# Kernel tuning notes

Measured on AMD Instinct MI355X. Metric: run time of the kernel, lower is better.

## Reference

```python
import jax, jax.numpy as jnp
import numpy as np

B, T, I, H, O = 8192, 512, 4, 32, 4


def setup_inputs() -> dict:
    key = jax.random.key(0)
    ks = jax.random.split(key, 11)
    s = 1.0 / np.sqrt(H)  # PyTorch RNN init scale
    return {
        "X": jax.random.normal(ks[0], (B, T, I), dtype=jnp.float32),
        "W_ih0": jax.random.uniform(ks[1], (H, I), minval=-s, maxval=s, dtype=jnp.float32),
        "W_hh0": jax.random.uniform(ks[2], (H, H), minval=-s, maxval=s, dtype=jnp.float32),
        "b_ih0": jax.random.uniform(ks[3], (H,), minval=-s, maxval=s, dtype=jnp.float32),
        "b_hh0": jax.random.uniform(ks[4], (H,), minval=-s, maxval=s, dtype=jnp.float32),
        "W_ih1": jax.random.uniform(ks[5], (H, H), minval=-s, maxval=s, dtype=jnp.float32),
        "W_hh1": jax.random.uniform(ks[6], (H, H), minval=-s, maxval=s, dtype=jnp.float32),
        "b_ih1": jax.random.uniform(ks[7], (H,), minval=-s, maxval=s, dtype=jnp.float32),
        "b_hh1": jax.random.uniform(ks[8], (H,), minval=-s, maxval=s, dtype=jnp.float32),
        "W_ll": jax.random.uniform(ks[9], (O, H), minval=-s, maxval=s, dtype=jnp.float32),
        "b_ll": jax.random.uniform(ks[10], (O,), minval=-s, maxval=s, dtype=jnp.float32),
    }


def reference(X, W_ih0, W_hh0, b_ih0, b_hh0, W_ih1, W_hh1, b_ih1, b_hh1, W_ll, b_ll):
    # 2-layer tanh RNN (batch_first), zero initial hidden state, then Linear head.
    b0 = b_ih0 + b_hh0
    b1 = b_ih1 + b_hh1
    Bsz = X.shape[0]
    Hdim = W_hh0.shape[0]
    h_init = (jnp.zeros((Bsz, Hdim), X.dtype), jnp.zeros((Bsz, Hdim), X.dtype))

    def step(h, x_t):
        h0, h1 = h
        h0 = jnp.tanh(x_t @ W_ih0.T + h0 @ W_hh0.T + b0)
        h1 = jnp.tanh(h0 @ W_ih1.T + h1 @ W_hh1.T + b1)
        return (h0, h1), h1

    xs = jnp.swapaxes(X, 0, 1)  # [T, B, I]
    _, ys = jax.lax.scan(step, h_init, xs)  # ys: [T, B, H]
    out = ys @ W_ll.T + b_ll  # [T, B, O]
    out = jnp.swapaxes(out, 0, 1)  # [B, T, O]
    return out.reshape(out.shape[0], -1)  # [B, T*O]
```

## Files before the change

### kernel.cpp

```cpp
#include <hip/hip_runtime.h>
#include <cstddef>
#include <cstdint>

constexpr int kB = 8192, kT = 512, kI = 4, kH = 32, kO = 4;

typedef _Float16 f16x8 __attribute__((ext_vector_type(8)));
typedef float    f32x4 __attribute__((ext_vector_type(4)));

#define MFMA(a, b, c) __builtin_amdgcn_mfma_f32_16x16x32_f16((a), (b), (c), 0, 0, 0)

__device__ __forceinline__ void bar_lds() {
    asm volatile("s_waitcnt lgkmcnt(0)" ::: "memory");
    __builtin_amdgcn_s_barrier();
    __builtin_amdgcn_sched_barrier(0);
}

__device__ __forceinline__ float fast_tanh(float x) {
    float e = __builtin_amdgcn_exp2f(x * 2.8853900817779268f);
    return 1.0f - 2.0f * __builtin_amdgcn_rcpf(e + 1.0f);
}

__device__ __forceinline__ float4 ld4(const float* p) { return *(const float4*)p; }

__device__ __forceinline__ f16x8 pack_frag(float4 lo, float4 hi) {
    f16x8 r;
    r[0] = (_Float16)lo.x; r[1] = (_Float16)lo.y;
    r[2] = (_Float16)lo.z; r[3] = (_Float16)lo.w;
    r[4] = (_Float16)hi.x; r[5] = (_Float16)hi.y;
    r[6] = (_Float16)hi.z; r[7] = (_Float16)hi.w;
    return r;
}

__device__ __forceinline__ f16x8 asm_frag(uint2 lo, uint2 hi) {
    union { f16x8 v; uint2 p[2]; } r;
    r.p[0] = lo; r.p[1] = hi;
    return r.v;
}

__device__ __forceinline__ uint2 pack_half(f32x4 t) {
    uint2 r;
    r.x = __builtin_bit_cast(uint32_t, __builtin_amdgcn_cvt_pkrtz(t[0], t[1]));
    r.y = __builtin_bit_cast(uint32_t, __builtin_amdgcn_cvt_pkrtz(t[2], t[3]));
    return r;
}

__device__ __forceinline__ f16x8 bxpack(float4 xn, bool g0) {
    union { f16x8 v; uint32_t u[4]; } bx;
    bx.u[0] = g0 ? __builtin_bit_cast(uint32_t, __builtin_amdgcn_cvt_pkrtz(xn.x, xn.y)) : 0u;
    bx.u[1] = g0 ? __builtin_bit_cast(uint32_t, __builtin_amdgcn_cvt_pkrtz(xn.z, xn.w)) : 0u;
    bx.u[2] = 0u; bx.u[3] = 0u;
    return bx.v;
}

__global__ __launch_bounds__(256, 2) void rnn2_quad(
    const float* __restrict__ X,
    const float* __restrict__ W_ih0, const float* __restrict__ W_hh0,
    const float* __restrict__ b_ih0, const float* __restrict__ b_hh0,
    const float* __restrict__ W_ih1, const float* __restrict__ W_hh1,
    const float* __restrict__ b_ih1, const float* __restrict__ b_hh1,
    const float* __restrict__ W_ll, const float* __restrict__ b_ll,
    float* __restrict__ out)
{
    const int  tid  = threadIdx.x;
    const int  wid  = tid >> 6;
    const int  half = wid & 1;
    const int  isB  = wid >> 1;
    const int  l    = tid & 63;
    const int  c    = l & 15;
    const int  g    = l >> 4;
    const bool g0   = (g == 0);
    const int  b    = blockIdx.x * 16 + c;
    const int  k0   = 4 * g;
    const int  ro   = half * 16;

    __shared__ uint2 h0buf[2][2][64];
    __shared__ uint2 h1buf[2][2][64];

    h0buf[tid >> 7][(tid >> 6) & 1][tid & 63] = make_uint2(0u, 0u);
    h1buf[tid >> 7][(tid >> 6) & 1][tid & 63] = make_uint2(0u, 0u);
    __syncthreads();

    const float4 z4 = make_float4(0.f, 0.f, 0.f, 0.f);

    if (isB == 0) {
        const float* wp = W_hh0 + (c + ro) * kH;
        const f16x8 Ahh = pack_frag(ld4(wp + k0), ld4(wp + 16 + k0));
        const f16x8 Aih = pack_frag(g0 ? ld4(W_ih0 + (c + ro) * kI) : z4, z4);
        f32x4 bias0;
#pragma unroll
        for (int r = 0; r < 4; ++r) bias0[r] = b_ih0[ro + k0 + r] + b_hh0[ro + k0 + r];

        uint2 myh = make_uint2(0u, 0u);
        f32x4 xc;
        const float* xp = X + (size_t)b * (kT * kI);

        float4 xv0 = ld4(xp);
        float4 xv1 = ld4(xp + 1 * kI);
        float4 xv2 = ld4(xp + 2 * kI);
        float4 xcur[4];
#pragma unroll
        for (int u = 0; u < 4; ++u) xcur[u] = ld4(xp + (3 + u) * kI);
        xc = MFMA(Aih, bxpack(xv0, g0), bias0);

        auto stepA = [&](float4 xn, int i) {
            const int rp = (i - 1) & 1, wpar = i & 1;
            uint2 sib = h0buf[rp][half ^ 1][l];
            f32x4 xcn = MFMA(Aih, bxpack(xn, g0), bias0);
            f16x8 Bh0 = half == 0 ? asm_frag(myh, sib) : asm_frag(sib, myh);
            f32x4 a = MFMA(Ahh, Bh0, xc);
            f32x4 t;
#pragma unroll
            for (int r = 0; r < 4; ++r) t[r] = fast_tanh(a[r]);
            myh = pack_half(t);
            h0buf[wpar][half][l] = myh;
            xc = xcn;
        };

        stepA(xv1, 0); bar_lds();
        stepA(xv2, 1); bar_lds();
        for (int tb = 0; tb < 128; ++tb) {
            const int i0 = 2 + tb * 4;
            float4 xnxt[4];
#pragma unroll
            for (int u = 0; u < 4; ++u) {
                int idx = i0 + 5 + u;
                idx = idx < kT ? idx : (kT - 1);
                xnxt[u] = ld4(xp + idx * kI);
            }
#pragma unroll
            for (int u = 0; u < 4; ++u) { stepA(xcur[u], i0 + u); bar_lds(); }
#pragma unroll
            for (int u = 0; u < 4; ++u) xcur[u] = xnxt[u];
        }
    } else {
        const float* wp = W_ih1 + (c + ro) * kH;
        const f16x8 Aih1 = pack_frag(ld4(wp + k0), ld4(wp + 16 + k0));
        wp = W_hh1 + (c + ro) * kH;
        const f16x8 Ahh1 = pack_frag(ld4(wp + k0), ld4(wp + 16 + k0));
        const f16x8 All = (half == 0 && c < kO)
            ? pack_frag(ld4(W_ll + c * kH + k0), ld4(W_ll + c * kH + 16 + k0))
            : pack_frag(z4, z4);

        f32x4 bias1, biasll;
#pragma unroll
        for (int r = 0; r < 4; ++r) {
            bias1[r]  = b_ih1[ro + k0 + r] + b_hh1[ro + k0 + r];
            biasll[r] = g0 ? b_ll[r] : 0.f;
        }

        uint2 myh1 = make_uint2(0u, 0u);
        float* op = out + (size_t)b * (kT * kO);

        auto stepB = [&](int i, bool store) {
            const int rp = (i - 1) & 1, wpar = i & 1;
            uint2 h0lo = h0buf[rp][0][l];
            uint2 h0hi = h0buf[rp][1][l];
            uint2 sib1 = h1buf[rp][half ^ 1][l];
            f16x8 Bh0 = asm_frag(h0lo, h0hi);
            f16x8 Bh1 = half == 0 ? asm_frag(myh1, sib1) : asm_frag(sib1, myh1);
            f32x4 o;
            if (half == 0) o = MFMA(All, Bh1, biasll);
            f32x4 cc = MFMA(Aih1, Bh0, bias1);
            cc = MFMA(Ahh1, Bh1, cc);
            f32x4 t;
#pragma unroll
            for (int r = 0; r < 4; ++r) t[r] = fast_tanh(cc[r]);
            myh1 = pack_half(t);
            h1buf[wpar][half][l] = myh1;
            if (store && half == 0 && g0)
                *(float4*)(op + (size_t)(i - 2) * kO) = make_float4(o[0], o[1], o[2], o[3]);
        };

        bar_lds();
        stepB(1, false); bar_lds();
        for (int tb = 0; tb < 128; ++tb) {
            const int i0 = 2 + tb * 4;
#pragma unroll
            for (int u = 0; u < 4; ++u) { stepB(i0 + u, true); bar_lds(); }
        }
    }
}

extern "C" void kernel_launch(void* const* d_in, const int* in_sizes, int n_in,
                              void* d_out, int out_size, void* d_ws, size_t ws_size,
                              hipStream_t stream) {
    const float* X     = (const float*)d_in[0];
    const float* W_ih0 = (const float*)d_in[1];
    const float* W_hh0 = (const float*)d_in[2];
    const float* b_ih0 = (const float*)d_in[3];
    const float* b_hh0 = (const float*)d_in[4];
    const float* W_ih1 = (const float*)d_in[5];
    const float* W_hh1 = (const float*)d_in[6];
    const float* b_ih1 = (const float*)d_in[7];
    const float* b_hh1 = (const float*)d_in[8];
    const float* W_ll  = (const float*)d_in[9];
    const float* b_ll  = (const float*)d_in[10];
    float* out = (float*)d_out;

    rnn2_quad<<<dim3(kB / 16), dim3(256), 0, stream>>>(
        X, W_ih0, W_hh0, b_ih0, b_hh0, W_ih1, W_hh1, b_ih1, b_hh1, W_ll, b_ll, out);
}
```

Measured before the change: 124.1 us.

## Interleave two batch tiles per block to overlap independent recurrence chains

Each block now processes 32 batch rows as two independent 16-row tiles. Every step interleaves the MFMAs, tanh and LDS exchanges of both tiles, so the two dependency chains can hide each other's latency inside one wave. This also halves the number of barriers per batch row. In exchange the grid is halved to one block per CU (launch bounds changed to 1), register and LDS use per block double, and the overlap that previously came from two co-resident blocks on a CU is given up.

```diff
diff --git a/kernel.cpp b/kernel.cpp
--- a/kernel.cpp
+++ b/kernel.cpp
@@ -52,7 +52,7 @@
     return bx.v;
 }
 
-__global__ __launch_bounds__(256, 2) void rnn2_quad(
+__global__ __launch_bounds__(256, 1) void rnn2_quad2(
     const float* __restrict__ X,
     const float* __restrict__ W_ih0, const float* __restrict__ W_hh0,
     const float* __restrict__ b_ih0, const float* __restrict__ b_hh0,
@@ -69,15 +69,20 @@
     const int  c    = l & 15;
     const int  g    = l >> 4;
     const bool g0   = (g == 0);
-    const int  b    = blockIdx.x * 16 + c;
+    const int  b0   = blockIdx.x * 32 + c;
+    const int  b1   = b0 + 16;
     const int  k0   = 4 * g;
     const int  ro   = half * 16;
 
-    __shared__ uint2 h0buf[2][2][64];
-    __shared__ uint2 h1buf[2][2][64];
-
-    h0buf[tid >> 7][(tid >> 6) & 1][tid & 63] = make_uint2(0u, 0u);
-    h1buf[tid >> 7][(tid >> 6) & 1][tid & 63] = make_uint2(0u, 0u);
+    __shared__ uint2 h0buf[2][2][2][64];
+    __shared__ uint2 h1buf[2][2][2][64];
+
+    {
+        uint2* p = (uint2*)h0buf;
+        uint2* q = (uint2*)h1buf;
+        p[tid] = make_uint2(0u, 0u); p[tid + 256] = make_uint2(0u, 0u);
+        q[tid] = make_uint2(0u, 0u); q[tid + 256] = make_uint2(0u, 0u);
+    }
     __syncthreads();
 
     const float4 z4 = make_float4(0.f, 0.f, 0.f, 0.f);
@@ -90,47 +95,59 @@
 #pragma unroll
         for (int r = 0; r < 4; ++r) bias0[r] = b_ih0[ro + k0 + r] + b_hh0[ro + k0 + r];
 
-        uint2 myh = make_uint2(0u, 0u);
-        f32x4 xc;
-        const float* xp = X + (size_t)b * (kT * kI);
-
-        float4 xv0 = ld4(xp);
-        float4 xv1 = ld4(xp + 1 * kI);
-        float4 xv2 = ld4(xp + 2 * kI);
-        float4 xcur[4];
-#pragma unroll
-        for (int u = 0; u < 4; ++u) xcur[u] = ld4(xp + (3 + u) * kI);
-        xc = MFMA(Aih, bxpack(xv0, g0), bias0);
-
-        auto stepA = [&](float4 xn, int i) {
+        uint2 m0 = make_uint2(0u, 0u), m1 = make_uint2(0u, 0u);
+        f32x4 xcA, xcB;
+        const float* xp0 = X + (size_t)b0 * (kT * kI);
+        const float* xp1 = X + (size_t)b1 * (kT * kI);
+
+        float4 xa0 = ld4(xp0), xb0 = ld4(xp1);
+        float4 xa1 = ld4(xp0 + 1 * kI), xb1 = ld4(xp1 + 1 * kI);
+        float4 xa2 = ld4(xp0 + 2 * kI), xb2 = ld4(xp1 + 2 * kI);
+        float4 xcur0[4], xcur1[4];
+#pragma unroll
+        for (int u = 0; u < 4; ++u) {
+            xcur0[u] = ld4(xp0 + (3 + u) * kI);
+            xcur1[u] = ld4(xp1 + (3 + u) * kI);
+        }
+        xcA = MFMA(Aih, bxpack(xa0, g0), bias0);
+        xcB = MFMA(Aih, bxpack(xb0, g0), bias0);
+
+        auto stepA = [&](float4 xn0, float4 xn1, int i) {
             const int rp = (i - 1) & 1, wpar = i & 1;
-            uint2 sib = h0buf[rp][half ^ 1][l];
-            f32x4 xcn = MFMA(Aih, bxpack(xn, g0), bias0);
-            f16x8 Bh0 = half == 0 ? asm_frag(myh, sib) : asm_frag(sib, myh);
-            f32x4 a = MFMA(Ahh, Bh0, xc);
-            f32x4 t;
-#pragma unroll
-            for (int r = 0; r < 4; ++r) t[r] = fast_tanh(a[r]);
-            myh = pack_half(t);
-            h0buf[wpar][half][l] = myh;
-            xc = xcn;
+            uint2 s0 = h0buf[0][rp][half ^ 1][l];
+            uint2 s1 = h0buf[1][rp][half ^ 1][l];
+            f32x4 xcn0 = MFMA(Aih, bxpack(xn0, g0), bias0);
+            f32x4 xcn1 = MFMA(Aih, bxpack(xn1, g0), bias0);
+            f16x8 B0 = half == 0 ? asm_frag(m0, s0) : asm_frag(s0, m0);
+            f32x4 a0 = MFMA(Ahh, B0, xcA);
+            f16x8 B1 = half == 0 ? asm_frag(m1, s1) : asm_frag(s1, m1);
+            f32x4 a1 = MFMA(Ahh, B1, xcB);
+            f32x4 t0, t1;
+#pragma unroll
+            for (int r = 0; r < 4; ++r) t0[r] = fast_tanh(a0[r]);
+#pragma unroll
+            for (int r = 0; r < 4; ++r) t1[r] = fast_tanh(a1[r]);
+            m0 = pack_half(t0); h0buf[0][wpar][half][l] = m0;
+            m1 = pack_half(t1); h0buf[1][wpar][half][l] = m1;
+            xcA = xcn0; xcB = xcn1;
         };
 
-        stepA(xv1, 0); bar_lds();
-        stepA(xv2, 1); bar_lds();
+        stepA(xa1, xb1, 0); bar_lds();
+        stepA(xa2, xb2, 1); bar_lds();
         for (int tb = 0; tb < 128; ++tb) {
             const int i0 = 2 + tb * 4;
-            float4 xnxt[4];
+            float4 xn0[4], xn1[4];
 #pragma unroll
             for (int u = 0; u < 4; ++u) {
                 int idx = i0 + 5 + u;
                 idx = idx < kT ? idx : (kT - 1);
-                xnxt[u] = ld4(xp + idx * kI);
+                xn0[u] = ld4(xp0 + idx * kI);
+                xn1[u] = ld4(xp1 + idx * kI);
             }
 #pragma unroll
-            for (int u = 0; u < 4; ++u) { stepA(xcur[u], i0 + u); bar_lds(); }
-#pragma unroll
-            for (int u = 0; u < 4; ++u) xcur[u] = xnxt[u];
+            for (int u = 0; u < 4; ++u) { stepA(xcur0[u], xcur1[u], i0 + u); bar_lds(); }
+#pragma unroll
+            for (int u = 0; u < 4; ++u) { xcur0[u] = xn0[u]; xcur1[u] = xn1[u]; }
         }
     } else {
         const float* wp = W_ih1 + (c + ro) * kH;
@@ -148,27 +165,38 @@
             biasll[r] = g0 ? b_ll[r] : 0.f;
         }
 
-        uint2 myh1 = make_uint2(0u, 0u);
-        float* op = out + (size_t)b * (kT * kO);
+        uint2 m0 = make_uint2(0u, 0u), m1 = make_uint2(0u, 0u);
+        float* op0 = out + (size_t)b0 * (kT * kO);
+        float* op1 = out + (size_t)b1 * (kT * kO);
 
         auto stepB = [&](int i, bool store) {
             const int rp = (i - 1) & 1, wpar = i & 1;
-            uint2 h0lo = h0buf[rp][0][l];
-            uint2 h0hi = h0buf[rp][1][l];
-            uint2 sib1 = h1buf[rp][half ^ 1][l];
-            f16x8 Bh0 = asm_frag(h0lo, h0hi);
-            f16x8 Bh1 = half == 0 ? asm_frag(myh1, sib1) : asm_frag(sib1, myh1);
-            f32x4 o;
-            if (half == 0) o = MFMA(All, Bh1, biasll);
-            f32x4 cc = MFMA(Aih1, Bh0, bias1);
-            cc = MFMA(Ahh1, Bh1, cc);
-            f32x4 t;
-#pragma unroll
-            for (int r = 0; r < 4; ++r) t[r] = fast_tanh(cc[r]);
-            myh1 = pack_half(t);
-            h1buf[wpar][half][l] = myh1;
-            if (store && half == 0 && g0)
-                *(float4*)(op + (size_t)(i - 2) * kO) = make_float4(o[0], o[1], o[2], o[3]);
+            uint2 h0lo0 = h0buf[0][rp][0][l], h0hi0 = h0buf[0][rp][1][l];
+            uint2 h0lo1 = h0buf[1][rp][0][l], h0hi1 = h0buf[1][rp][1][l];
+            uint2 s10 = h1buf[0][rp][half ^ 1][l];
+            uint2 s11 = h1buf[1][rp][half ^ 1][l];
+            f16x8 Bh1_0 = half == 0 ? asm_frag(m0, s10) : asm_frag(s10, m0);
+            f32x4 o0;
+            if (half == 0) o0 = MFMA(All, Bh1_0, biasll);
+            f32x4 cc0 = MFMA(Aih1, asm_frag(h0lo0, h0hi0), bias1);
+            cc0 = MFMA(Ahh1, Bh1_0, cc0);
+            f16x8 Bh1_1 = half == 0 ? asm_frag(m1, s11) : asm_frag(s11, m1);
+            f32x4 o1;
+            if (half == 0) o1 = MFMA(All, Bh1_1, biasll);
+            f32x4 cc1 = MFMA(Aih1, asm_frag(h0lo1, h0hi1), bias1);
+            cc1 = MFMA(Ahh1, Bh1_1, cc1);
+
+            f32x4 t0, t1;
+#pragma unroll
+            for (int r = 0; r < 4; ++r) t0[r] = fast_tanh(cc0[r]);
+#pragma unroll
+            for (int r = 0; r < 4; ++r) t1[r] = fast_tanh(cc1[r]);
+            m0 = pack_half(t0); h1buf[0][wpar][half][l] = m0;
+            m1 = pack_half(t1); h1buf[1][wpar][half][l] = m1;
+            if (store && half == 0 && g0) {
+                *(float4*)(op0 + (size_t)(i - 2) * kO) = make_float4(o0[0], o0[1], o0[2], o0[3]);
+                *(float4*)(op1 + (size_t)(i - 2) * kO) = make_float4(o1[0], o1[1], o1[2], o1[3]);
+            }
         };
 
         bar_lds();
@@ -197,6 +225,6 @@
     const float* b_ll  = (const float*)d_in[10];
     float* out = (float*)d_out;
 
-    rnn2_quad<<<dim3(kB / 16), dim3(256), 0, stream>>>(
+    rnn2_quad2<<<dim3(kB / 32), dim3(256), 0, stream>>>(
         X, W_ih0, W_hh0, b_ih0, b_hh0, W_ih1, W_hh1, b_ih1, b_hh1, W_ll, b_ll, out);
 }
```

New measurement: 168.7 us. +35.9%, slower.
